# Kernel optimization log

Measured on AMD Instinct MI355X. Metric: run time of the kernel, lower is better.

## Reference

```python
import jax, jax.numpy as jnp
import numpy as np

N = 200000   # total nodes across batched graphs
E = 800000   # total edges
B = 4096     # number of graphs
IN = 32      # node feature dim
H1 = 128
D = 64       # set2set / conv3 dim


def setup_inputs():
    key = jax.random.key(0)
    ks = jax.random.split(key, 36)
    def rn(k, shape, s=0.05):
        return jax.random.normal(k, shape, dtype=jnp.float32) * s
    inp = {}
    inp["x"] = jax.random.normal(ks[0], (N, IN), dtype=jnp.float32)
    inp["edge_attr"] = jax.random.uniform(ks[1], (E, 6), dtype=jnp.float32)
    inp["t"] = jax.random.uniform(ks[2], (B, 1), dtype=jnp.float32)
    inp["p"] = jax.random.uniform(ks[3], (B, 1), dtype=jnp.float32)
    inp["e1_w"] = rn(ks[4], (6, IN));    inp["e1_b"] = rn(ks[5], (IN,))
    inp["nn1_w"] = rn(ks[6], (IN, H1));  inp["nn1_b"] = rn(ks[7], (H1,))
    inp["l1_w"] = rn(ks[8], (IN, H1));   inp["l1_b"] = rn(ks[9], (H1,))
    inp["e2_w"] = rn(ks[10], (6, H1));   inp["e2_b"] = rn(ks[11], (H1,))
    inp["nn2_w"] = rn(ks[12], (H1, H1)); inp["nn2_b"] = rn(ks[13], (H1,))
    inp["l2_w"] = rn(ks[14], (H1, H1));  inp["l2_b"] = rn(ks[15], (H1,))
    inp["e3_w"] = rn(ks[16], (6, H1));   inp["e3_b"] = rn(ks[17], (H1,))
    inp["nn3_w"] = rn(ks[18], (H1, D));  inp["nn3_b"] = rn(ks[19], (D,))
    inp["l3_w"] = rn(ks[20], (H1, D));   inp["l3_b"] = rn(ks[21], (D,))
    inp["lstm_wih"] = rn(ks[22], (2 * D, 4 * D))
    inp["lstm_whh"] = rn(ks[23], (D, 4 * D))
    inp["lstm_bih"] = rn(ks[24], (4 * D,))
    inp["lstm_bhh"] = rn(ks[25], (4 * D,))
    inp["l4_w"] = rn(ks[26], (2 * D + 2, H1)); inp["l4_b"] = rn(ks[27], (H1,))
    inp["l5_w"] = rn(ks[28], (H1, 1));         inp["l5_b"] = rn(ks[29], (1,))
    inp["edge_index"] = jax.random.randint(ks[30], (2, E), 0, N)
    inp["batch"] = jnp.sort(jax.random.randint(ks[31], (N,), 0, B))
    inp["num_graphs"] = B
    return inp


def _gine(x, edge_index, edge_attr, ew, eb, nw, nb):
    # PyG GINEConv with eps=0: nn((1+eps)*x_i + sum_j relu(x_j + edge_lin(e_ji)))
    src, dst = edge_index[0], edge_index[1]
    msg = jax.nn.relu(x[src] + edge_attr @ ew + eb)               # [E, d]
    aggr = jax.ops.segment_sum(msg, dst, num_segments=x.shape[0])  # [N, d]
    return (x + aggr) @ nw + nb


def _set2set(x, batch, num_graphs, wih, whh, bih, bhh, steps=3):
    d = x.shape[1]
    h = jnp.zeros((num_graphs, d), x.dtype)
    c = jnp.zeros((num_graphs, d), x.dtype)
    q_star = jnp.zeros((num_graphs, 2 * d), x.dtype)
    for _ in range(steps):
        # single-step LSTM (torch gate order i, f, g, o)
        gates = q_star @ wih + h @ whh + bih + bhh
        i, f, g, o = jnp.split(gates, 4, axis=1)
        c = jax.nn.sigmoid(f) * c + jax.nn.sigmoid(i) * jnp.tanh(g)
        h = jax.nn.sigmoid(o) * jnp.tanh(c)
        q = h
        # segment-wise softmax attention over nodes of each graph
        e = jnp.sum(x * q[batch], axis=1)                           # [N]
        emax = jax.ops.segment_max(e, batch, num_segments=num_graphs)
        a = jnp.exp(e - emax[batch])
        asum = jax.ops.segment_sum(a, batch, num_segments=num_graphs)
        a = a / asum[batch]
        r = jax.ops.segment_sum(a[:, None] * x, batch, num_segments=num_graphs)
        q_star = jnp.concatenate([q, r], axis=1)
    return q_star


def reference(x, edge_attr, t, p, e1_w, e1_b, nn1_w, nn1_b, l1_w, l1_b, e2_w, e2_b, nn2_w, nn2_b, l2_w, l2_b, e3_w, e3_b, nn3_w, nn3_b, l3_w, l3_b, lstm_wih, lstm_whh, lstm_bih, lstm_bhh, l4_w, l4_b, l5_w, l5_b, edge_index, batch, num_graphs):
    h = jax.nn.elu(_gine(x, edge_index, edge_attr, e1_w, e1_b, nn1_w, nn1_b) + x @ l1_w + l1_b)
    h = jax.nn.elu(_gine(h, edge_index, edge_attr, e2_w, e2_b, nn2_w, nn2_b) + h @ l2_w + l2_b)
    h = _gine(h, edge_index, edge_attr, e3_w, e3_b, nn3_w, nn3_b) + h @ l3_w + l3_b
    out = _set2set(h, batch, num_graphs, lstm_wih, lstm_whh, lstm_bih, lstm_bhh)
    out = jnp.concatenate([out, t, p], axis=1)  # [B, 130]
    out = jax.nn.relu(out @ l4_w + l4_b)
    out = out @ l5_w + l5_b
    return out.reshape(-1)
```

## Files before the change

kernel.cpp:

```cpp
#include <hip/hip_runtime.h>
#include <hip/hip_bf16.h>
#include <math.h>

#define DEV __device__ __forceinline__
using u16 = unsigned short;
typedef __attribute__((ext_vector_type(8))) short bf16x8;
typedef __attribute__((ext_vector_type(4))) float f32x4;

DEV float elu1(float x) { return x > 0.f ? x : expm1f(x); }
DEV float sigm(float x) { return 1.f / (1.f + expf(-x)); }
DEV float b2f(u16 v) { return __uint_as_float((unsigned)v << 16); }
DEV u16 f2b(float x) { __hip_bfloat16 b = __float2bfloat16(x); return *reinterpret_cast<u16*>(&b); }

__global__ __launch_bounds__(256) void deg_hist(const int* __restrict__ ei,
                                                int* __restrict__ deg, int E) {
    const int e = blockIdx.x * 256 + threadIdx.x;
    if (e < E) atomicAdd(&deg[ei[E + e]], 1);
}

__global__ __launch_bounds__(256) void scan1(const int* __restrict__ deg,
                                             int* __restrict__ part,
                                             int* __restrict__ bsum, int N) {
    __shared__ int lds[256];
    const int t = threadIdx.x;
    const int base = blockIdx.x * 1024;
    int v[4]; int s = 0;
    #pragma unroll
    for (int k = 0; k < 4; ++k) {
        const int idx = base + t * 4 + k;
        v[k] = (idx < N) ? deg[idx] : 0;
        s += v[k];
    }
    lds[t] = s; __syncthreads();
    int incl = s;
    for (int off = 1; off < 256; off <<= 1) {
        const int add = (t >= off) ? lds[t - off] : 0;
        __syncthreads();
        incl += add; lds[t] = incl;
        __syncthreads();
    }
    if (t == 255) bsum[blockIdx.x] = incl;
    int run = incl - s;
    #pragma unroll
    for (int k = 0; k < 4; ++k) {
        const int idx = base + t * 4 + k;
        if (idx < N) part[idx] = run;
        run += v[k];
    }
}

__global__ __launch_bounds__(256) void scan2(int* __restrict__ bsum, int nb) {
    __shared__ int lds[256];
    __shared__ int carry;
    const int t = threadIdx.x;
    if (t == 0) carry = 0;
    __syncthreads();
    for (int base = 0; base < nb; base += 256) {
        const int idx = base + t;
        const int v = (idx < nb) ? bsum[idx] : 0;
        lds[t] = v; __syncthreads();
        int incl = v;
        for (int off = 1; off < 256; off <<= 1) {
            const int add = (t >= off) ? lds[t - off] : 0;
            __syncthreads();
            incl += add; lds[t] = incl;
            __syncthreads();
        }
        const int c = carry;
        if (idx < nb) bsum[idx] = c + incl - v;
        __syncthreads();
        if (t == 255) carry = c + incl;
        __syncthreads();
    }
}

__global__ __launch_bounds__(256) void scan3(const int* __restrict__ part,
                                             const int* __restrict__ bsum,
                                             int* __restrict__ rowstart,
                                             int* __restrict__ cursor, int N, int E) {
    const int i = blockIdx.x * 256 + threadIdx.x;
    if (i < N) {
        const int v = part[i] + bsum[i >> 10];
        rowstart[i] = v;
        cursor[i] = v;
    }
    if (i == 0) rowstart[N] = E;
}

__global__ __launch_bounds__(256) void edge_scatter(const int* __restrict__ ei,
                                                    const float* __restrict__ eattr,
                                                    int* __restrict__ cursor,
                                                    int* __restrict__ src_s,
                                                    float* __restrict__ eattr_s, int E) {
    const int e = blockIdx.x * 256 + threadIdx.x;
    if (e >= E) return;
    const int src = ei[e], dst = ei[E + e];
    const float2 a0 = *(const float2*)(eattr + (size_t)e * 6);
    const float2 a1 = *(const float2*)(eattr + (size_t)e * 6 + 2);
    const float2 a2 = *(const float2*)(eattr + (size_t)e * 6 + 4);
    const int pos = atomicAdd(&cursor[dst], 1);
    src_s[pos] = src;
    float* ds = eattr_s + (size_t)pos * 6;
    *(float2*)ds = a0; *(float2*)(ds + 2) = a1; *(float2*)(ds + 4) = a2;
}

__global__ __launch_bounds__(256) void build_gstart(const int* __restrict__ batch,
                                                    int* __restrict__ gstart, int N, int B) {
    const int i = blockIdx.x * 256 + threadIdx.x;
    if (i >= N) return;
    const int b = batch[i];
    if (i == 0) for (int g = 0; g <= b; ++g) gstart[g] = 0;
    else {
        const int pb = batch[i - 1];
        for (int g = pb + 1; g <= b; ++g) gstart[g] = i;
    }
    if (i == N - 1) for (int g = b + 1; g <= B; ++g) gstart[g] = N;
}

template<int DIN, int DOUT>
__global__ __launch_bounds__(256) void wcat_prep(
    const float* __restrict__ nnW, const float* __restrict__ lW,
    const float* __restrict__ nnB, const float* __restrict__ lB,
    u16* __restrict__ wswz, float* __restrict__ bcomb)
{
    constexpr int COLT = DOUT / 16;
    const int idx = blockIdx.x * 256 + threadIdx.x;
    if (idx < 2 * DIN * DOUT) {
        const int k = idx / DOUT, n = idx % DOUT;
        const float v = (k < DIN) ? nnW[k * DOUT + n]
                                  : nnW[(k - DIN) * DOUT + n] + lW[(k - DIN) * DOUT + n];
        const int kc = k >> 5, khi = (k >> 3) & 3, j = k & 7;
        const int ct = n >> 4, n16 = n & 15;
        wswz[(size_t)(((kc * COLT + ct) * 4 + khi) * 16 + n16) * 8 + j] = f2b(v);
    }
    if (idx < DOUT) bcomb[idx] = nnB[idx] + lB[idx];
}

__global__ __launch_bounds__(256) void f32_to_bf16v(const float* __restrict__ src,
                                                    u16* __restrict__ dst, int n4) {
    const int i = blockIdx.x * 256 + threadIdx.x;
    if (i >= n4) return;
    const float4 v = *(const float4*)(src + (size_t)i * 4);
    ushort4 u; u.x = f2b(v.x); u.y = f2b(v.y); u.z = f2b(v.z); u.w = f2b(v.w);
    *(ushort4*)(dst + (size_t)i * 4) = u;
}

__global__ __launch_bounds__(256) void edge_gather32(
    const float* __restrict__ xin, const float* __restrict__ eattr_s,
    const float* __restrict__ ew, const float* __restrict__ eb,
    const int* __restrict__ rowstart, const int* __restrict__ src_s,
    u16* __restrict__ agg, int N)
{
    const int tid = threadIdx.x;
    const int j = tid & 31;
    const int n = blockIdx.x * 8 + (tid >> 5);
    if (n >= N) return;
    const float w0 = ew[0 * 32 + j], w1 = ew[1 * 32 + j], w2 = ew[2 * 32 + j],
                w3 = ew[3 * 32 + j], w4 = ew[4 * 32 + j], w5 = ew[5 * 32 + j];
    const float bj = eb[j];
    const int s0 = rowstart[n], s1 = rowstart[n + 1];
    float accA = 0.f, accB = 0.f;
    int k = s0;
    for (; k + 4 <= s1; k += 4) {
        int sr[4];
        #pragma unroll
        for (int u = 0; u < 4; ++u) sr[u] = src_s[k + u];
        float xv[4]; float2 ea[4][3];
        #pragma unroll
        for (int u = 0; u < 4; ++u) {
            xv[u] = xin[(size_t)sr[u] * 32 + j];
            const float* ep = eattr_s + (size_t)(k + u) * 6;
            ea[u][0] = *(const float2*)ep;
            ea[u][1] = *(const float2*)(ep + 2);
            ea[u][2] = *(const float2*)(ep + 4);
        }
        #pragma unroll
        for (int u = 0; u < 4; ++u) {
            float el = bj;
            el = fmaf(ea[u][0].x, w0, el); el = fmaf(ea[u][0].y, w1, el);
            el = fmaf(ea[u][1].x, w2, el); el = fmaf(ea[u][1].y, w3, el);
            el = fmaf(ea[u][2].x, w4, el); el = fmaf(ea[u][2].y, w5, el);
            const float m = fmaxf(xv[u] + el, 0.f);
            if (u & 1) accB += m; else accA += m;
        }
    }
    for (; k < s1; ++k) {
        const int sr = src_s[k];
        const float* ep = eattr_s + (size_t)k * 6;
        float el = bj;
        el = fmaf(ep[0], w0, el); el = fmaf(ep[1], w1, el);
        el = fmaf(ep[2], w2, el); el = fmaf(ep[3], w3, el);
        el = fmaf(ep[4], w4, el); el = fmaf(ep[5], w5, el);
        accA += fmaxf(xin[(size_t)sr * 32 + j] + el, 0.f);
    }
    agg[(size_t)n * 32 + j] = f2b(accA + accB);
}

__global__ __launch_bounds__(256) void edge_gather128(
    const u16* __restrict__ xin, const float* __restrict__ eattr_s,
    const float* __restrict__ ew, const float* __restrict__ eb,
    const int* __restrict__ rowstart, const int* __restrict__ src_s,
    u16* __restrict__ agg, int N)
{
    const int lane = threadIdx.x & 63;
    int n = blockIdx.x * 4 + (threadIdx.x >> 6);
    n = __builtin_amdgcn_readfirstlane(n);
    if (n >= N) return;
    const int j0 = lane << 1;
    float2 wv[6];
    #pragma unroll
    for (int q = 0; q < 6; ++q) wv[q] = *(const float2*)(ew + q * 128 + j0);
    const float2 bv = *(const float2*)(eb + j0);
    const int s0 = rowstart[n], s1 = rowstart[n + 1];
    float a0A = 0.f, a1A = 0.f, a0B = 0.f, a1B = 0.f;
    int k = s0;
    for (; k + 4 <= s1; k += 4) {
        int sr[4];
        #pragma unroll
        for (int u = 0; u < 4; ++u) sr[u] = src_s[k + u];
        ushort2 xv[4];
        #pragma unroll
        for (int u = 0; u < 4; ++u)
            xv[u] = *(const ushort2*)(xin + (size_t)sr[u] * 128 + j0);
        #pragma unroll
        for (int u = 0; u < 4; ++u) {
            const float* ep = eattr_s + (size_t)(k + u) * 6;
            const float e0 = ep[0], e1 = ep[1], e2 = ep[2], e3 = ep[3], e4 = ep[4], e5 = ep[5];
            float l0 = bv.x, l1 = bv.y;
            l0 = fmaf(e0, wv[0].x, l0); l1 = fmaf(e0, wv[0].y, l1);
            l0 = fmaf(e1, wv[1].x, l0); l1 = fmaf(e1, wv[1].y, l1);
            l0 = fmaf(e2, wv[2].x, l0); l1 = fmaf(e2, wv[2].y, l1);
            l0 = fmaf(e3, wv[3].x, l0); l1 = fmaf(e3, wv[3].y, l1);
            l0 = fmaf(e4, wv[4].x, l0); l1 = fmaf(e4, wv[4].y, l1);
            l0 = fmaf(e5, wv[5].x, l0); l1 = fmaf(e5, wv[5].y, l1);
            const float m0 = fmaxf(b2f(xv[u].x) + l0, 0.f);
            const float m1 = fmaxf(b2f(xv[u].y) + l1, 0.f);
            if (u & 1) { a0B += m0; a1B += m1; } else { a0A += m0; a1A += m1; }
        }
    }
    for (; k < s1; ++k) {
        const int sr = src_s[k];
        const ushort2 xv = *(const ushort2*)(xin + (size_t)sr * 128 + j0);
        const float* ep = eattr_s + (size_t)k * 6;
        float l0 = bv.x, l1 = bv.y;
        l0 = fmaf(ep[0], wv[0].x, l0); l1 = fmaf(ep[0], wv[0].y, l1);
        l0 = fmaf(ep[1], wv[1].x, l0); l1 = fmaf(ep[1], wv[1].y, l1);
        l0 = fmaf(ep[2], wv[2].x, l0); l1 = fmaf(ep[2], wv[2].y, l1);
        l0 = fmaf(ep[3], wv[3].x, l0); l1 = fmaf(ep[3], wv[3].y, l1);
        l0 = fmaf(ep[4], wv[4].x, l0); l1 = fmaf(ep[4], wv[4].y, l1);
        l0 = fmaf(ep[5], wv[5].x, l0); l1 = fmaf(ep[5], wv[5].y, l1);
        a0A += fmaxf(b2f(xv.x) + l0, 0.f);
        a1A += fmaxf(b2f(xv.y) + l1, 0.f);
    }
    ushort2 o; o.x = f2b(a0A + a0B); o.y = f2b(a1A + a1B);
    *(ushort2*)(agg + (size_t)n * 128 + j0) = o;
}

template<int DIN, int DOUT, bool ELU, typename TOUT>
__global__ __launch_bounds__(256) void node_update_mfma(
    const u16* __restrict__ aggb, const u16* __restrict__ xb,
    const u16* __restrict__ wswz, const float* __restrict__ bcomb,
    TOUT* __restrict__ out, int N)
{
    constexpr int KC1    = DIN / 32;
    constexpr int KC_TOT = 2 * KC1;
    constexpr int COLT   = DOUT / 16;
    const int l  = threadIdx.x & 63;
    const int w  = threadIdx.x >> 6;
    const int nb = (blockIdx.x * 4 + w) * 16;
    if (nb >= N) return;
    const int n16 = l & 15, khi = l >> 4;
    const int arow = min(nb + n16, N - 1);
    f32x4 acc[COLT];
    #pragma unroll
    for (int ct = 0; ct < COLT; ++ct) acc[ct] = (f32x4){0.f, 0.f, 0.f, 0.f};
    const u16* abase = aggb + (size_t)arow * DIN + khi * 8;
    const u16* xbase = xb   + (size_t)arow * DIN + khi * 8;
    #pragma unroll
    for (int kc = 0; kc < KC_TOT; ++kc) {
        const u16* ap = (kc < KC1) ? (abase + kc * 32) : (xbase + (kc - KC1) * 32);
        const bf16x8 af = *(const bf16x8*)ap;
        #pragma unroll
        for (int ct = 0; ct < COLT; ++ct) {
            const bf16x8 bf = *(const bf16x8*)(wswz + (size_t)(((kc * COLT + ct) * 4 + khi) * 16 + n16) * 8);
            acc[ct] = __builtin_amdgcn_mfma_f32_16x16x32_bf16(af, bf, acc[ct], 0, 0, 0);
        }
    }
    #pragma unroll
    for (int ct = 0; ct < COLT; ++ct) {
        const int col = ct * 16 + n16;
        const float bv = bcomb[col];
        #pragma unroll
        for (int r = 0; r < 4; ++r) {
            const int node = nb + khi * 4 + r;
            if (node < N) {
                float v = acc[ct][r] + bv;
                if (ELU) v = elu1(v);
                if constexpr (sizeof(TOUT) == 2) out[(size_t)node * DOUT + col] = (TOUT)f2b(v);
                else                             out[(size_t)node * DOUT + col] = (TOUT)v;
            }
        }
    }
}

__global__ __launch_bounds__(256) void lstm_gates(
    const float* __restrict__ qstar, const float* __restrict__ hS,
    const float* __restrict__ wih, const float* __restrict__ whh,
    const float* __restrict__ bih, const float* __restrict__ bhh,
    float* __restrict__ gates, int B)
{
    const int idx = blockIdx.x * 256 + threadIdx.x;
    const int g = idx >> 8, jj = idx & 255;
    if (g >= B) return;
    float acc = bih[jj] + bhh[jj];
    const float* q = qstar + g * 128;
    const float* h = hS + g * 64;
    #pragma unroll 4
    for (int k = 0; k < 128; ++k) acc = fmaf(q[k], wih[k * 256 + jj], acc);
    #pragma unroll 4
    for (int k = 0; k < 64;  ++k) acc = fmaf(h[k], whh[k * 256 + jj], acc);
    gates[g * 256 + jj] = acc;
}

__global__ __launch_bounds__(256) void lstm_update(
    const float* __restrict__ gates, float* __restrict__ cS, float* __restrict__ hS, int B)
{
    const int idx = blockIdx.x * 256 + threadIdx.x;
    const int g = idx >> 6, d = idx & 63;
    if (g >= B) return;
    const float i_ = gates[g * 256 + d];
    const float f_ = gates[g * 256 + 64 + d];
    const float g_ = gates[g * 256 + 128 + d];
    const float o_ = gates[g * 256 + 192 + d];
    float c = cS[g * 64 + d];
    c = sigm(f_) * c + sigm(i_) * tanhf(g_);
    cS[g * 64 + d] = c;
    hS[g * 64 + d] = sigm(o_) * tanhf(c);
}

__global__ __launch_bounds__(256) void attn_step(
    const float* __restrict__ h3, const float* __restrict__ hS,
    const int* __restrict__ gstart, float* __restrict__ qstar, int B)
{
    const int g = (blockIdx.x * 256 + threadIdx.x) >> 6;
    const int lane = threadIdx.x & 63;
    if (g >= B) return;
    const float q = hS[g * 64 + lane];
    const int s0 = gstart[g], s1 = gstart[g + 1];
    float m = -INFINITY, ssum = 0.f, racc = 0.f;
    for (int n = s0; n < s1; ++n) {
        const float hv = h3[(size_t)n * 64 + lane];
        float v = hv * q;
        #pragma unroll
        for (int off = 32; off; off >>= 1) v += __shfl_xor(v, off, 64);
        const float mnew = fmaxf(m, v);
        const float sc = expf(m - mnew);
        const float a  = expf(v - mnew);
        ssum = ssum * sc + a;
        racc = racc * sc + a * hv;
        m = mnew;
    }
    const float r = (ssum > 0.f) ? racc / ssum : 0.f;
    qstar[g * 128 + lane] = q;
    qstar[g * 128 + 64 + lane] = r;
}

__global__ __launch_bounds__(256) void mlp_hidden(
    const float* __restrict__ qstar, const float* __restrict__ t, const float* __restrict__ p,
    const float* __restrict__ l4w, const float* __restrict__ l4b,
    float* __restrict__ hidden, int B)
{
    const int idx = blockIdx.x * 256 + threadIdx.x;
    const int g = idx >> 7, j = idx & 127;
    if (g >= B) return;
    float acc = l4b[j];
    const float* q = qstar + g * 128;
    #pragma unroll 4
    for (int k = 0; k < 128; ++k) acc = fmaf(q[k], l4w[k * 128 + j], acc);
    acc = fmaf(t[g], l4w[128 * 128 + j], acc);
    acc = fmaf(p[g], l4w[129 * 128 + j], acc);
    hidden[g * 128 + j] = fmaxf(acc, 0.f);
}

__global__ __launch_bounds__(256) void out_proj(
    const float* __restrict__ hidden, const float* __restrict__ l5w,
    const float* __restrict__ l5b, float* __restrict__ dout, int B)
{
    const int wid = (blockIdx.x * 256 + threadIdx.x) >> 6;
    const int lane = threadIdx.x & 63;
    if (wid >= B) return;
    float s = fmaf(hidden[wid * 128 + lane], l5w[lane],
                   hidden[wid * 128 + 64 + lane] * l5w[64 + lane]);
    #pragma unroll
    for (int m = 32; m; m >>= 1) s += __shfl_xor(s, m, 64);
    if (lane == 0) dout[wid] = s + l5b[0];
}

extern "C" void kernel_launch(void* const* d_in, const int* in_sizes, int n_in,
                              void* d_out, int out_size, void* d_ws, size_t ws_size,
                              hipStream_t stream)
{
    const float* x     = (const float*)d_in[0];
    const float* eattr = (const float*)d_in[1];
    const float* t     = (const float*)d_in[2];
    const float* p     = (const float*)d_in[3];
    const float* e1w = (const float*)d_in[4];  const float* e1b = (const float*)d_in[5];
    const float* nn1w= (const float*)d_in[6];  const float* nn1b= (const float*)d_in[7];
    const float* l1w = (const float*)d_in[8];  const float* l1b = (const float*)d_in[9];
    const float* e2w = (const float*)d_in[10]; const float* e2b = (const float*)d_in[11];
    const float* nn2w= (const float*)d_in[12]; const float* nn2b= (const float*)d_in[13];
    const float* l2w = (const float*)d_in[14]; const float* l2b = (const float*)d_in[15];
    const float* e3w = (const float*)d_in[16]; const float* e3b = (const float*)d_in[17];
    const float* nn3w= (const float*)d_in[18]; const float* nn3b= (const float*)d_in[19];
    const float* l3w = (const float*)d_in[20]; const float* l3b = (const float*)d_in[21];
    const float* wih = (const float*)d_in[22]; const float* whh = (const float*)d_in[23];
    const float* bih = (const float*)d_in[24]; const float* bhh = (const float*)d_in[25];
    const float* l4w = (const float*)d_in[26]; const float* l4b = (const float*)d_in[27];
    const float* l5w = (const float*)d_in[28]; const float* l5b = (const float*)d_in[29];
    const int* ei    = (const int*)d_in[30];
    const int* batch = (const int*)d_in[31];
    float* dout = (float*)d_out;

    const int N = in_sizes[0] / 32;
    const int E = in_sizes[30] / 2;
    const int B = in_sizes[2];

    char* basep = (char*)d_ws;
    size_t off = 0;
    auto take = [&](size_t bytes) -> char* {
        char* ptr = basep + off;
        off = (off + bytes + 255) & ~(size_t)255;
        return ptr;
    };
    int* src_s      = (int*)  take((size_t)E * 4);
    float* eattr_s  = (float*)take((size_t)E * 24);
    int* deg      = (int*) take((size_t)N * 4);
    int* part     = (int*) take((size_t)N * 4);
    int* bsum     = (int*) take(4096);
    int* rowstart = (int*) take((size_t)(N + 1) * 4);
    int* cursor   = (int*) take((size_t)N * 4);
    int* gstart   = (int*) take((size_t)(B + 1) * 4);
    u16* aggr     = (u16*) take((size_t)N * 128 * 2);
    u16* h1       = (u16*) take((size_t)N * 128 * 2);
    u16* h2       = (u16*) take((size_t)N * 128 * 2);
    float* h3     = (float*)h1;
    u16* xb       = (u16*) take((size_t)N * 32 * 2);
    u16* w1swz    = (u16*) take((size_t)2 * 32 * 128 * 2);
    u16* w2swz    = (u16*) take((size_t)2 * 128 * 128 * 2);
    u16* w3swz    = (u16*) take((size_t)2 * 128 * 64 * 2);
    float* b1c    = (float*)take(128 * 4);
    float* b2c    = (float*)take(128 * 4);
    float* b3c    = (float*)take(64 * 4);
    float* hS     = (float*)take((size_t)B * 256 * 4);
    float* cS     = hS + (size_t)B * 64;
    float* qstar  = cS + (size_t)B * 64;
    float* gates  = (float*)take((size_t)B * 256 * 4);
    float* hidden = (float*)take((size_t)B * 128 * 4);
    (void)ws_size;

    hipMemsetAsync(deg, 0, (size_t)N * 4, stream);
    deg_hist<<<(E + 255) / 256, 256, 0, stream>>>(ei, deg, E);
    const int NB1 = (N + 1023) / 1024;
    scan1<<<NB1, 256, 0, stream>>>(deg, part, bsum, N);
    scan2<<<1, 256, 0, stream>>>(bsum, NB1);
    scan3<<<(N + 255) / 256, 256, 0, stream>>>(part, bsum, rowstart, cursor, N, E);
    edge_scatter<<<(E + 255) / 256, 256, 0, stream>>>(ei, eattr, cursor, src_s, eattr_s, E);
    build_gstart<<<(N + 255) / 256, 256, 0, stream>>>(batch, gstart, N, B);
    f32_to_bf16v<<<(N * 8 + 255) / 256, 256, 0, stream>>>(x, xb, N * 8);
    wcat_prep<32, 128><<<(2 * 32 * 128 + 255) / 256, 256, 0, stream>>>(nn1w, l1w, nn1b, l1b, w1swz, b1c);
    wcat_prep<128, 128><<<(2 * 128 * 128 + 255) / 256, 256, 0, stream>>>(nn2w, l2w, nn2b, l2b, w2swz, b2c);
    wcat_prep<128, 64><<<(2 * 128 * 64 + 255) / 256, 256, 0, stream>>>(nn3w, l3w, nn3b, l3b, w3swz, b3c);

    edge_gather32<<<(N + 7) / 8, 256, 0, stream>>>(
        x, eattr_s, e1w, e1b, rowstart, src_s, aggr, N);
    node_update_mfma<32, 128, true, u16><<<(N + 63) / 64, 256, 0, stream>>>(
        aggr, xb, w1swz, b1c, h1, N);

    edge_gather128<<<(N + 3) / 4, 256, 0, stream>>>(
        h1, eattr_s, e2w, e2b, rowstart, src_s, aggr, N);
    node_update_mfma<128, 128, true, u16><<<(N + 63) / 64, 256, 0, stream>>>(
        aggr, h1, w2swz, b2c, h2, N);

    edge_gather128<<<(N + 3) / 4, 256, 0, stream>>>(
        h2, eattr_s, e3w, e3b, rowstart, src_s, aggr, N);
    node_update_mfma<128, 64, false, float><<<(N + 63) / 64, 256, 0, stream>>>(
        aggr, h2, w3swz, b3c, h3, N);

    hipMemsetAsync(hS, 0, (size_t)B * 256 * 4, stream);
    for (int step = 0; step < 3; ++step) {
        lstm_gates<<<(B * 256 + 255) / 256, 256, 0, stream>>>(qstar, hS, wih, whh, bih, bhh, gates, B);
        lstm_update<<<(B * 64 + 255) / 256, 256, 0, stream>>>(gates, cS, hS, B);
        attn_step<<<(B * 64 + 255) / 256, 256, 0, stream>>>(h3, hS, gstart, qstar, B);
    }

    mlp_hidden<<<(B * 128 + 255) / 256, 256, 0, stream>>>(qstar, t, p, l4w, l4b, hidden, B);
    out_proj<<<(B * 64 + 255) / 256, 256, 0, stream>>>(hidden, l5w, l5b, dout, B);
}
```

Baseline: 721.7 us.

## Fuse edge aggregation with MFMA node update per 64-node tile via LDS

Each GINE layer's edge gather and node-update GEMM now run in one kernel. The aggregated tile for 64 nodes is held in shared memory and fed straight to MFMA, so the global aggr buffer round trip and one launch per layer go away. Output is staged through LDS for coalesced float4 stores. The set2set attention loop is also unrolled by two nodes so two shuffle reductions overlap. The cost is fewer, larger blocks with 17KB of LDS and tail imbalance inside a block from skewed degrees.

```diff
diff --git a/kernel.cpp b/kernel.cpp
--- a/kernel.cpp
+++ b/kernel.cpp
@@ -145,161 +145,189 @@
     *(ushort4*)(dst + (size_t)i * 4) = u;
 }
 
-__global__ __launch_bounds__(256) void edge_gather32(
-    const float* __restrict__ xin, const float* __restrict__ eattr_s,
-    const float* __restrict__ ew, const float* __restrict__ eb,
+template<int DIN, int DOUT, bool ELU, typename TOUT>
+__global__ __launch_bounds__(256) void fused_layer(
+    const float* __restrict__ xf,
+    const u16* __restrict__ hb,
+    const float* __restrict__ eattr_s, const float* __restrict__ ew, const float* __restrict__ eb,
     const int* __restrict__ rowstart, const int* __restrict__ src_s,
-    u16* __restrict__ agg, int N)
-{
-    const int tid = threadIdx.x;
-    const int j = tid & 31;
-    const int n = blockIdx.x * 8 + (tid >> 5);
-    if (n >= N) return;
-    const float w0 = ew[0 * 32 + j], w1 = ew[1 * 32 + j], w2 = ew[2 * 32 + j],
-                w3 = ew[3 * 32 + j], w4 = ew[4 * 32 + j], w5 = ew[5 * 32 + j];
-    const float bj = eb[j];
-    const int s0 = rowstart[n], s1 = rowstart[n + 1];
-    float accA = 0.f, accB = 0.f;
-    int k = s0;
-    for (; k + 4 <= s1; k += 4) {
-        int sr[4];
-        #pragma unroll
-        for (int u = 0; u < 4; ++u) sr[u] = src_s[k + u];
-        float xv[4]; float2 ea[4][3];
-        #pragma unroll
-        for (int u = 0; u < 4; ++u) {
-            xv[u] = xin[(size_t)sr[u] * 32 + j];
-            const float* ep = eattr_s + (size_t)(k + u) * 6;
-            ea[u][0] = *(const float2*)ep;
-            ea[u][1] = *(const float2*)(ep + 2);
-            ea[u][2] = *(const float2*)(ep + 4);
-        }
-        #pragma unroll
-        for (int u = 0; u < 4; ++u) {
-            float el = bj;
-            el = fmaf(ea[u][0].x, w0, el); el = fmaf(ea[u][0].y, w1, el);
-            el = fmaf(ea[u][1].x, w2, el); el = fmaf(ea[u][1].y, w3, el);
-            el = fmaf(ea[u][2].x, w4, el); el = fmaf(ea[u][2].y, w5, el);
-            const float m = fmaxf(xv[u] + el, 0.f);
-            if (u & 1) accB += m; else accA += m;
-        }
-    }
-    for (; k < s1; ++k) {
-        const int sr = src_s[k];
-        const float* ep = eattr_s + (size_t)k * 6;
-        float el = bj;
-        el = fmaf(ep[0], w0, el); el = fmaf(ep[1], w1, el);
-        el = fmaf(ep[2], w2, el); el = fmaf(ep[3], w3, el);
-        el = fmaf(ep[4], w4, el); el = fmaf(ep[5], w5, el);
-        accA += fmaxf(xin[(size_t)sr * 32 + j] + el, 0.f);
-    }
-    agg[(size_t)n * 32 + j] = f2b(accA + accB);
-}
-
-__global__ __launch_bounds__(256) void edge_gather128(
-    const u16* __restrict__ xin, const float* __restrict__ eattr_s,
-    const float* __restrict__ ew, const float* __restrict__ eb,
-    const int* __restrict__ rowstart, const int* __restrict__ src_s,
-    u16* __restrict__ agg, int N)
-{
-    const int lane = threadIdx.x & 63;
-    int n = blockIdx.x * 4 + (threadIdx.x >> 6);
-    n = __builtin_amdgcn_readfirstlane(n);
-    if (n >= N) return;
-    const int j0 = lane << 1;
-    float2 wv[6];
-    #pragma unroll
-    for (int q = 0; q < 6; ++q) wv[q] = *(const float2*)(ew + q * 128 + j0);
-    const float2 bv = *(const float2*)(eb + j0);
-    const int s0 = rowstart[n], s1 = rowstart[n + 1];
-    float a0A = 0.f, a1A = 0.f, a0B = 0.f, a1B = 0.f;
-    int k = s0;
-    for (; k + 4 <= s1; k += 4) {
-        int sr[4];
-        #pragma unroll
-        for (int u = 0; u < 4; ++u) sr[u] = src_s[k + u];
-        ushort2 xv[4];
-        #pragma unroll
-        for (int u = 0; u < 4; ++u)
-            xv[u] = *(const ushort2*)(xin + (size_t)sr[u] * 128 + j0);
-        #pragma unroll
-        for (int u = 0; u < 4; ++u) {
-            const float* ep = eattr_s + (size_t)(k + u) * 6;
-            const float e0 = ep[0], e1 = ep[1], e2 = ep[2], e3 = ep[3], e4 = ep[4], e5 = ep[5];
-            float l0 = bv.x, l1 = bv.y;
-            l0 = fmaf(e0, wv[0].x, l0); l1 = fmaf(e0, wv[0].y, l1);
-            l0 = fmaf(e1, wv[1].x, l0); l1 = fmaf(e1, wv[1].y, l1);
-            l0 = fmaf(e2, wv[2].x, l0); l1 = fmaf(e2, wv[2].y, l1);
-            l0 = fmaf(e3, wv[3].x, l0); l1 = fmaf(e3, wv[3].y, l1);
-            l0 = fmaf(e4, wv[4].x, l0); l1 = fmaf(e4, wv[4].y, l1);
-            l0 = fmaf(e5, wv[5].x, l0); l1 = fmaf(e5, wv[5].y, l1);
-            const float m0 = fmaxf(b2f(xv[u].x) + l0, 0.f);
-            const float m1 = fmaxf(b2f(xv[u].y) + l1, 0.f);
-            if (u & 1) { a0B += m0; a1B += m1; } else { a0A += m0; a1A += m1; }
-        }
-    }
-    for (; k < s1; ++k) {
-        const int sr = src_s[k];
-        const ushort2 xv = *(const ushort2*)(xin + (size_t)sr * 128 + j0);
-        const float* ep = eattr_s + (size_t)k * 6;
-        float l0 = bv.x, l1 = bv.y;
-        l0 = fmaf(ep[0], wv[0].x, l0); l1 = fmaf(ep[0], wv[0].y, l1);
-        l0 = fmaf(ep[1], wv[1].x, l0); l1 = fmaf(ep[1], wv[1].y, l1);
-        l0 = fmaf(ep[2], wv[2].x, l0); l1 = fmaf(ep[2], wv[2].y, l1);
-        l0 = fmaf(ep[3], wv[3].x, l0); l1 = fmaf(ep[3], wv[3].y, l1);
-        l0 = fmaf(ep[4], wv[4].x, l0); l1 = fmaf(ep[4], wv[4].y, l1);
-        l0 = fmaf(ep[5], wv[5].x, l0); l1 = fmaf(ep[5], wv[5].y, l1);
-        a0A += fmaxf(b2f(xv.x) + l0, 0.f);
-        a1A += fmaxf(b2f(xv.y) + l1, 0.f);
-    }
-    ushort2 o; o.x = f2b(a0A + a0B); o.y = f2b(a1A + a1B);
-    *(ushort2*)(agg + (size_t)n * 128 + j0) = o;
-}
-
-template<int DIN, int DOUT, bool ELU, typename TOUT>
-__global__ __launch_bounds__(256) void node_update_mfma(
-    const u16* __restrict__ aggb, const u16* __restrict__ xb,
     const u16* __restrict__ wswz, const float* __restrict__ bcomb,
     TOUT* __restrict__ out, int N)
 {
-    constexpr int KC1    = DIN / 32;
+    constexpr int KC1  = DIN / 32;
     constexpr int KC_TOT = 2 * KC1;
-    constexpr int COLT   = DOUT / 16;
-    const int l  = threadIdx.x & 63;
-    const int w  = threadIdx.x >> 6;
-    const int nb = (blockIdx.x * 4 + w) * 16;
-    if (nb >= N) return;
-    const int n16 = l & 15, khi = l >> 4;
-    const int arow = min(nb + n16, N - 1);
-    f32x4 acc[COLT];
-    #pragma unroll
-    for (int ct = 0; ct < COLT; ++ct) acc[ct] = (f32x4){0.f, 0.f, 0.f, 0.f};
-    const u16* abase = aggb + (size_t)arow * DIN + khi * 8;
-    const u16* xbase = xb   + (size_t)arow * DIN + khi * 8;
+    constexpr int COLT = DOUT / 16;
+    constexpr int CTW  = COLT / 4;
+    constexpr int ASTR = (DIN == 32) ? 80 : 272;
+    __shared__ char ldsb[64 * 272];
+    const int tid = threadIdx.x;
+    const int nb  = blockIdx.x * 64;
+
+    if constexpr (DIN == 32) {
+        const int j = tid & 31;
+        const float w0 = ew[j], w1 = ew[32 + j], w2 = ew[64 + j],
+                    w3 = ew[96 + j], w4 = ew[128 + j], w5 = ew[160 + j];
+        const float bj = eb[j];
+        #pragma unroll 2
+        for (int it = 0; it < 8; ++it) {
+            const int nl = it * 8 + (tid >> 5);
+            const int n = nb + nl;
+            if (n < N) {
+                const int s0 = rowstart[n], s1 = rowstart[n + 1];
+                float accA = 0.f, accB = 0.f;
+                int k = s0;
+                for (; k + 4 <= s1; k += 4) {
+                    int sr[4];
+                    #pragma unroll
+                    for (int u = 0; u < 4; ++u) sr[u] = src_s[k + u];
+                    float xv[4]; float2 ea[4][3];
+                    #pragma unroll
+                    for (int u = 0; u < 4; ++u) {
+                        xv[u] = xf[(size_t)sr[u] * 32 + j];
+                        const float* ep = eattr_s + (size_t)(k + u) * 6;
+                        ea[u][0] = *(const float2*)ep;
+                        ea[u][1] = *(const float2*)(ep + 2);
+                        ea[u][2] = *(const float2*)(ep + 4);
+                    }
+                    #pragma unroll
+                    for (int u = 0; u < 4; ++u) {
+                        float el = bj;
+                        el = fmaf(ea[u][0].x, w0, el); el = fmaf(ea[u][0].y, w1, el);
+                        el = fmaf(ea[u][1].x, w2, el); el = fmaf(ea[u][1].y, w3, el);
+                        el = fmaf(ea[u][2].x, w4, el); el = fmaf(ea[u][2].y, w5, el);
+                        const float m = fmaxf(xv[u] + el, 0.f);
+                        if (u & 1) accB += m; else accA += m;
+                    }
+                }
+                for (; k < s1; ++k) {
+                    const int sr = src_s[k];
+                    const float* ep = eattr_s + (size_t)k * 6;
+                    float el = bj;
+                    el = fmaf(ep[0], w0, el); el = fmaf(ep[1], w1, el);
+                    el = fmaf(ep[2], w2, el); el = fmaf(ep[3], w3, el);
+                    el = fmaf(ep[4], w4, el); el = fmaf(ep[5], w5, el);
+                    accA += fmaxf(xf[(size_t)sr * 32 + j] + el, 0.f);
+                }
+                *(u16*)(ldsb + nl * 80 + j * 2) = f2b(accA + accB);
+            }
+        }
+    } else {
+        const int lane = tid & 63;
+        const int wid  = tid >> 6;
+        const int j0 = lane << 1;
+        float2 wv[6];
+        #pragma unroll
+        for (int q = 0; q < 6; ++q) wv[q] = *(const float2*)(ew + q * 128 + j0);
+        const float2 bv = *(const float2*)(eb + j0);
+        for (int it = 0; it < 16; ++it) {
+            const int n = __builtin_amdgcn_readfirstlane(nb + it * 4 + wid);
+            const int nl = n - nb;
+            if (n < N) {
+                const int s0 = rowstart[n], s1 = rowstart[n + 1];
+                float a0A = 0.f, a1A = 0.f, a0B = 0.f, a1B = 0.f;
+                int k = s0;
+                for (; k + 4 <= s1; k += 4) {
+                    int sr[4];
+                    #pragma unroll
+                    for (int u = 0; u < 4; ++u) sr[u] = src_s[k + u];
+                    ushort2 xv[4];
+                    #pragma unroll
+                    for (int u = 0; u < 4; ++u)
+                        xv[u] = *(const ushort2*)(hb + (size_t)sr[u] * 128 + j0);
+                    #pragma unroll
+                    for (int u = 0; u < 4; ++u) {
+                        const float* ep = eattr_s + (size_t)(k + u) * 6;
+                        const float e0 = ep[0], e1 = ep[1], e2 = ep[2],
+                                    e3 = ep[3], e4 = ep[4], e5 = ep[5];
+                        float l0 = bv.x, l1 = bv.y;
+                        l0 = fmaf(e0, wv[0].x, l0); l1 = fmaf(e0, wv[0].y, l1);
+                        l0 = fmaf(e1, wv[1].x, l0); l1 = fmaf(e1, wv[1].y, l1);
+                        l0 = fmaf(e2, wv[2].x, l0); l1 = fmaf(e2, wv[2].y, l1);
+                        l0 = fmaf(e3, wv[3].x, l0); l1 = fmaf(e3, wv[3].y, l1);
+                        l0 = fmaf(e4, wv[4].x, l0); l1 = fmaf(e4, wv[4].y, l1);
+                        l0 = fmaf(e5, wv[5].x, l0); l1 = fmaf(e5, wv[5].y, l1);
+                        const float m0 = fmaxf(b2f(xv[u].x) + l0, 0.f);
+                        const float m1 = fmaxf(b2f(xv[u].y) + l1, 0.f);
+                        if (u & 1) { a0B += m0; a1B += m1; } else { a0A += m0; a1A += m1; }
+                    }
+                }
+                for (; k < s1; ++k) {
+                    const int sr = src_s[k];
+                    const ushort2 xv = *(const ushort2*)(hb + (size_t)sr * 128 + j0);
+                    const float* ep = eattr_s + (size_t)k * 6;
+                    float l0 = bv.x, l1 = bv.y;
+                    l0 = fmaf(ep[0], wv[0].x, l0); l1 = fmaf(ep[0], wv[0].y, l1);
+                    l0 = fmaf(ep[1], wv[1].x, l0); l1 = fmaf(ep[1], wv[1].y, l1);
+                    l0 = fmaf(ep[2], wv[2].x, l0); l1 = fmaf(ep[2], wv[2].y, l1);
+                    l0 = fmaf(ep[3], wv[3].x, l0); l1 = fmaf(ep[3], wv[3].y, l1);
+                    l0 = fmaf(ep[4], wv[4].x, l0); l1 = fmaf(ep[4], wv[4].y, l1);
+                    l0 = fmaf(ep[5], wv[5].x, l0); l1 = fmaf(ep[5], wv[5].y, l1);
+                    a0A += fmaxf(b2f(xv.x) + l0, 0.f);
+                    a1A += fmaxf(b2f(xv.y) + l1, 0.f);
+                }
+                ushort2 o; o.x = f2b(a0A + a0B); o.y = f2b(a1A + a1B);
+                *(ushort2*)(ldsb + nl * 272 + j0 * 2) = o;
+            }
+        }
+    }
+    __syncthreads();
+
+    const int lane = tid & 63, wid = tid >> 6;
+    const int n16 = lane & 15, khi = lane >> 4;
+    f32x4 acc[4][CTW];
+    #pragma unroll
+    for (int g = 0; g < 4; ++g)
+        #pragma unroll
+        for (int c = 0; c < CTW; ++c) acc[g][c] = (f32x4){0.f, 0.f, 0.f, 0.f};
     #pragma unroll
     for (int kc = 0; kc < KC_TOT; ++kc) {
-        const u16* ap = (kc < KC1) ? (abase + kc * 32) : (xbase + (kc - KC1) * 32);
-        const bf16x8 af = *(const bf16x8*)ap;
-        #pragma unroll
-        for (int ct = 0; ct < COLT; ++ct) {
-            const bf16x8 bf = *(const bf16x8*)(wswz + (size_t)(((kc * COLT + ct) * 4 + khi) * 16 + n16) * 8);
-            acc[ct] = __builtin_amdgcn_mfma_f32_16x16x32_bf16(af, bf, acc[ct], 0, 0, 0);
-        }
-    }
-    #pragma unroll
-    for (int ct = 0; ct < COLT; ++ct) {
-        const int col = ct * 16 + n16;
+        bf16x8 bf[CTW];
+        #pragma unroll
+        for (int c = 0; c < CTW; ++c) {
+            const int ct = wid * CTW + c;
+            bf[c] = *(const bf16x8*)(wswz + (size_t)(((kc * COLT + ct) * 4 + khi) * 16 + n16) * 8);
+        }
+        #pragma unroll
+        for (int g = 0; g < 4; ++g) {
+            bf16x8 af;
+            if (kc < KC1) {
+                af = *(const bf16x8*)(ldsb + (g * 16 + n16) * ASTR + kc * 64 + khi * 16);
+            } else {
+                const int row = min(nb + g * 16 + n16, N - 1);
+                af = *(const bf16x8*)(hb + (size_t)row * DIN + (kc - KC1) * 32 + khi * 8);
+            }
+            #pragma unroll
+            for (int c = 0; c < CTW; ++c)
+                acc[g][c] = __builtin_amdgcn_mfma_f32_16x16x32_bf16(af, bf[c], acc[g][c], 0, 0, 0);
+        }
+    }
+    __syncthreads();
+
+    #pragma unroll
+    for (int c = 0; c < CTW; ++c) {
+        const int col = (wid * CTW + c) * 16 + n16;
         const float bv = bcomb[col];
         #pragma unroll
-        for (int r = 0; r < 4; ++r) {
-            const int node = nb + khi * 4 + r;
-            if (node < N) {
-                float v = acc[ct][r] + bv;
+        for (int g = 0; g < 4; ++g) {
+            #pragma unroll
+            for (int r = 0; r < 4; ++r) {
+                const int nl = g * 16 + khi * 4 + r;
+                float v = acc[g][c][r] + bv;
                 if (ELU) v = elu1(v);
-                if constexpr (sizeof(TOUT) == 2) out[(size_t)node * DOUT + col] = (TOUT)f2b(v);
-                else                             out[(size_t)node * DOUT + col] = (TOUT)v;
+                if constexpr (sizeof(TOUT) == 2) *(u16*)(ldsb + nl * 272 + col * 2) = f2b(v);
+                else                             *(float*)(ldsb + nl * 272 + col * 4) = v;
             }
         }
+    }
+    __syncthreads();
+    char* outc = (char*)out;
+    #pragma unroll
+    for (int it = 0; it < 4; ++it) {
+        const int task = it * 256 + tid;
+        const int row = task >> 4, cch = task & 15;
+        if (nb + row < N)
+            *(float4*)(outc + (size_t)(nb + row) * (DOUT * sizeof(TOUT)) + cch * 16) =
+                *(const float4*)(ldsb + row * 272 + cch * 16);
     }
 }
 
@@ -348,7 +376,25 @@
     const float q = hS[g * 64 + lane];
     const int s0 = gstart[g], s1 = gstart[g + 1];
     float m = -INFINITY, ssum = 0.f, racc = 0.f;
-    for (int n = s0; n < s1; ++n) {
+    int n = s0;
+    for (; n + 2 <= s1; n += 2) {
+        const float hv0 = h3[(size_t)n * 64 + lane];
+        const float hv1 = h3[(size_t)(n + 1) * 64 + lane];
+        float v0 = hv0 * q, v1 = hv1 * q;
+        #pragma unroll
+        for (int off = 32; off; off >>= 1) {
+            v0 += __shfl_xor(v0, off, 64);
+            v1 += __shfl_xor(v1, off, 64);
+        }
+        const float mnew = fmaxf(m, fmaxf(v0, v1));
+        const float sc = expf(m - mnew);
+        const float a0 = expf(v0 - mnew);
+        const float a1 = expf(v1 - mnew);
+        ssum = ssum * sc + a0 + a1;
+        racc = racc * sc + a0 * hv0 + a1 * hv1;
+        m = mnew;
+    }
+    for (; n < s1; ++n) {
         const float hv = h3[(size_t)n * 64 + lane];
         float v = hv * q;
         #pragma unroll
@@ -440,7 +486,6 @@
     int* rowstart = (int*) take((size_t)(N + 1) * 4);
     int* cursor   = (int*) take((size_t)N * 4);
     int* gstart   = (int*) take((size_t)(B + 1) * 4);
-    u16* aggr     = (u16*) take((size_t)N * 128 * 2);
     u16* h1       = (u16*) take((size_t)N * 128 * 2);
     u16* h2       = (u16*) take((size_t)N * 128 * 2);
     float* h3     = (float*)h1;
@@ -471,20 +516,13 @@
     wcat_prep<128, 128><<<(2 * 128 * 128 + 255) / 256, 256, 0, stream>>>(nn2w, l2w, nn2b, l2b, w2swz, b2c);
     wcat_prep<128, 64><<<(2 * 128 * 64 + 255) / 256, 256, 0, stream>>>(nn3w, l3w, nn3b, l3b, w3swz, b3c);
 
-    edge_gather32<<<(N + 7) / 8, 256, 0, stream>>>(
-        x, eattr_s, e1w, e1b, rowstart, src_s, aggr, N);
-    node_update_mfma<32, 128, true, u16><<<(N + 63) / 64, 256, 0, stream>>>(
-        aggr, xb, w1swz, b1c, h1, N);
-
-    edge_gather128<<<(N + 3) / 4, 256, 0, stream>>>(
-        h1, eattr_s, e2w, e2b, rowstart, src_s, aggr, N);
-    node_update_mfma<128, 128, true, u16><<<(N + 63) / 64, 256, 0, stream>>>(
-        aggr, h1, w2swz, b2c, h2, N);
-
-    edge_gather128<<<(N + 3) / 4, 256, 0, stream>>>(
-        h2, eattr_s, e3w, e3b, rowstart, src_s, aggr, N);
-    node_update_mfma<128, 64, false, float><<<(N + 63) / 64, 256, 0, stream>>>(
-        aggr, h2, w3swz, b3c, h3, N);
+    const int FB = (N + 63) / 64;
+    fused_layer<32, 128, true, u16><<<FB, 256, 0, stream>>>(
+        x, xb, eattr_s, e1w, e1b, rowstart, src_s, w1swz, b1c, h1, N);
+    fused_layer<128, 128, true, u16><<<FB, 256, 0, stream>>>(
+        nullptr, h1, eattr_s, e2w, e2b, rowstart, src_s, w2swz, b2c, h2, N);
+    fused_layer<128, 64, false, float><<<FB, 256, 0, stream>>>(
+        nullptr, h2, eattr_s, e3w, e3b, rowstart, src_s, w3swz, b3c, h3, N);
 
     hipMemsetAsync(hS, 0, (size_t)B * 256 * 4, stream);
     for (int step = 0; step < 3; ++step) {
```

Result: faster. 645.6 us (-10.5%).
